# Kernel tuning notes

Measured on AMD Instinct MI355X. Metric: run time of the kernel, lower is better.

The kernel has to match this reference:

```python
import jax, jax.numpy as jnp
import numpy as np

T = 8
TAU = 2.0       # spikingjelly LIFNode default tau
VTH = 1.0       # default v_threshold
ALPHA = 2.0     # surrogate.ATan alpha
EPS = 1e-5      # BatchNorm eps


@jax.custom_vjp
def spike_fn(x):
    # Heaviside with ATan surrogate gradient
    return (x >= 0.0).astype(x.dtype)

def _spike_fwd(x):
    return (x >= 0.0).astype(x.dtype), x

def _spike_bwd(x, g):
    sg = (ALPHA / 2.0) / (1.0 + (jnp.pi / 2.0 * ALPHA * x) ** 2)
    return (g * sg,)

spike_fn.defvjp(_spike_fwd, _spike_bwd)


def lif(x_seq):
    """Multi-step LIF over leading time axis. decay_input=True, hard reset to 0, detach_reset."""
    def step(v, x):
        v = v + (x - v) / TAU            # charge
        s = spike_fn(v - VTH)            # fire (surrogate grad)
        v = v * (1.0 - jax.lax.stop_gradient(s))  # detached hard reset to v_reset=0
        return v, s
    _, s_seq = jax.lax.scan(step, jnp.zeros_like(x_seq[0]), x_seq)
    return s_seq


def conv2d(x, w, b, stride):
    y = jax.lax.conv_general_dilated(x, w, (stride, stride), 'VALID',
                                     dimension_numbers=('NCHW', 'OIHW', 'NCHW'))
    return y + b[None, :, None, None]


def batchnorm(x, g, b):
    # training-mode BN over merged (T*B, H, W) axes, matching step_mode='m' BatchNorm2d
    m = x.mean((0, 2, 3), keepdims=True)
    v = x.var((0, 2, 3), keepdims=True)
    return g[None, :, None, None] * (x - m) * jax.lax.rsqrt(v + EPS) + b[None, :, None, None]


def setup_inputs() -> dict:
    key = jax.random.key(0)
    ks = jax.random.split(key, 12)
    def w_init(k, shape):
        fan_in = int(np.prod(shape[1:]))
        return jax.random.normal(k, shape, dtype=jnp.float32) / np.sqrt(fan_in)
    x = jax.random.normal(ks[0], (128, 4, 84, 84), dtype=jnp.float32)
    return {
        'x': x,
        'conv1_w': w_init(ks[1], (32, 4, 8, 8)),  'conv1_b': jnp.zeros((32,), jnp.float32),
        'bn1_g': jnp.ones((32,), jnp.float32),    'bn1_b': jnp.zeros((32,), jnp.float32),
        'conv2_w': w_init(ks[2], (64, 32, 4, 4)), 'conv2_b': jnp.zeros((64,), jnp.float32),
        'bn2_g': jnp.ones((64,), jnp.float32),    'bn2_b': jnp.zeros((64,), jnp.float32),
        'conv3_w': w_init(ks[3], (64, 64, 3, 3)), 'conv3_b': jnp.zeros((64,), jnp.float32),
        'bn3_g': jnp.ones((64,), jnp.float32),    'bn3_b': jnp.zeros((64,), jnp.float32),
        'fc1_w': w_init(ks[4], (512, 3136)),      'fc1_b': jnp.zeros((512,), jnp.float32),
        'fco_w': w_init(ks[5], (2, 512)),         'fco_b': jnp.zeros((2,), jnp.float32),
    }


def reference(x, conv1_w, conv1_b, bn1_g, bn1_b, conv2_w, conv2_b, bn2_g, bn2_b,
              conv3_w, conv3_b, bn3_g, bn3_b, fc1_w, fc1_b, fco_w, fco_b):
    B = x.shape[0]
    # replicate input over T timesteps; fold T into batch for conv/BN (step_mode='m')
    xs = jnp.broadcast_to(x, (T,) + x.shape).reshape((T * B,) + x.shape[1:])

    h = batchnorm(conv2d(xs, conv1_w, conv1_b, 4), bn1_g, bn1_b)   # [TB,32,20,20]
    s = lif(h.reshape((T, B) + h.shape[1:]))
    h = s.reshape((T * B,) + s.shape[2:])

    h = batchnorm(conv2d(h, conv2_w, conv2_b, 2), bn2_g, bn2_b)    # [TB,64,9,9]
    s = lif(h.reshape((T, B) + h.shape[1:]))
    h = s.reshape((T * B,) + s.shape[2:])

    h = batchnorm(conv2d(h, conv3_w, conv3_b, 1), bn3_g, bn3_b)    # [TB,64,7,7]
    s = lif(h.reshape((T, B) + h.shape[1:]))                        # [T,B,64,7,7]

    feat = s.reshape(T, B, -1)                                      # [T,B,3136]
    hid = lif(jnp.einsum('tbi,oi->tbo', feat, fc1_w) + fc1_b)       # [T,B,512]
    out_seq = jnp.einsum('tbo,ko->tbk', hid, fco_w) + fco_b         # [T,B,2]
    return out_seq.mean(0)                                          # [B,2]
```

## Files before the change

### kernel.cpp

```cpp
#include <hip/hip_runtime.h>
#include <cstdint>
#include <cstddef>

#define TT 8

#define E2_ELEMS (128*64*81)
#define E3_ELEMS (128*64*49)

typedef __attribute__((ext_vector_type(8))) short short8;
typedef __attribute__((ext_vector_type(4))) float f32x4;

#define BAR_LDS() do { asm volatile("s_waitcnt lgkmcnt(0)" ::: "memory"); \
                       __builtin_amdgcn_s_barrier(); } while (0)

__device__ __forceinline__ void gld_lds16(const void* g, void* l) {
  __builtin_amdgcn_global_load_lds((const __attribute__((address_space(1))) void*)g,
                                   (__attribute__((address_space(3))) void*)l, 16, 0, 0);
}

__global__ void prep_all(const float* __restrict__ w1, const float* __restrict__ w2,
                         const float* __restrict__ w3, float* __restrict__ wT1,
                         __bf16* __restrict__ w2f, __bf16* __restrict__ w3f) {
  int i = blockIdx.x * 256 + threadIdx.x;
  if (i < 8192) {
    int oc = i >> 8, pos = i & 255;
    wT1[(oc >> 4) * 4096 + pos * 16 + (oc & 15)] = w1[oc * 256 + pos];
  } else if (i < 106496) {
    int v = i - 8192;
    int j    = v & 7;
    int oc   = (v >> 3) & 63;
    int quad = (v >> 9) & 3;
    int ksg  = (v >> 11) & 15;
    int term = v >> 15;
    int k = ksg * 32 + quad * 8 + j;
    int ci = k >> 4, kpos = k & 15;
    float w = w2[oc * 512 + ci * 16 + kpos];
    float hf = (float)(__bf16)w;
    float r1 = w - hf;
    float mf = (float)(__bf16)r1;
    float r2 = r1 - mf;
    w2f[v] = (term == 0) ? (__bf16)w : (term == 1) ? (__bf16)r1 : (__bf16)r2;
  } else if (i < 217088) {
    int v = i - 106496;
    int j    = v & 7;
    int oc   = (v >> 3) & 63;
    int quad = (v >> 9) & 3;
    int tk   = v >> 11;
    int term = tk / 18, kstep = tk % 18;
    int k = kstep * 32 + quad * 8 + j;
    int pos = k >> 6, ci = k & 63;
    float w = w3[oc * 576 + ci * 9 + pos];
    float hf = (float)(__bf16)w;
    float r1 = w - hf;
    float mf = (float)(__bf16)r1;
    float r2 = r1 - mf;
    w3f[v] = (term == 0) ? (__bf16)w : (term == 1) ? (__bf16)r1 : (__bf16)r2;
  }
}

__global__ __launch_bounds__(256) void prep_wff(const float* __restrict__ w,
                                                __bf16* __restrict__ wf) {
  __shared__ float tile[12544];
  int oc0 = blockIdx.x * 32;
  int ci0 = blockIdx.y * 8;
  int tid = threadIdx.x;
  for (int f = tid; f < 12544; f += 256) {
    int oc_l = f / 392, r = f - oc_l * 392;
    tile[f] = w[(size_t)(oc0 + oc_l) * 3136 + ci0 * 49 + r];
  }
  __syncthreads();
  int squad = (ci0 & 31) >> 3;
  int sadd  = ci0 >> 5;
  for (int g = tid; g < 1568; g += 256) {
    int pos = g >> 5, oc_l = g & 31;
    union { __bf16 h[8]; uint4 u; } T0, T1, T2;
    #pragma unroll
    for (int j = 0; j < 8; j++) {
      float wv = tile[oc_l * 392 + j * 49 + pos];
      float hf = (float)(__bf16)wv;
      float r1 = wv - hf;
      float mf = (float)(__bf16)r1;
      float r2 = r1 - mf;
      T0.h[j] = (__bf16)wv; T1.h[j] = (__bf16)r1; T2.h[j] = (__bf16)r2;
    }
    int s = pos * 2 + sadd;
    size_t b0 = (((size_t)s * 4 + squad) * 512 + oc0 + oc_l) * 8;
    *(uint4*)(wf + b0)           = T0.u;
    *(uint4*)(wf + b0 + 1605632) = T1.u;
    *(uint4*)(wf + b0 + 3211264) = T2.u;
  }
}

__global__ __launch_bounds__(128) void k_conv1(const float* __restrict__ x,
                                               const float* __restrict__ wT,
                                               const float* __restrict__ bias,
                                               float* __restrict__ out,
                                               float* __restrict__ pout) {
  __shared__ float xt[8064];
  int tid = threadIdx.x;
  int img = blockIdx.x >> 2;
  int q   = blockIdx.x & 3;
  int och = blockIdx.y;
  float4* dst = (float4*)xt;
  #pragma unroll
  for (int ci = 0; ci < 4; ci++) {
    const float4* s4 = (const float4*)(x + (size_t)img * 28224 + ci * 7056 + q * 1680);
    for (int i = tid; i < 504; i += 128) dst[ci * 504 + i] = s4[i];
  }
  __syncthreads();
  bool active = tid < 100;
  int oyl = tid / 20, ox = tid % 20;
  float acc[16];
  #pragma unroll
  for (int j = 0; j < 16; j++) acc[j] = 0.f;
  if (active) {
    int xb0 = oyl * 336 + ox * 4;
    const float* wh = wT + och * 4096;
    #pragma unroll 1
    for (int ci = 0; ci < 4; ci++) {
      #pragma unroll 1
      for (int ky = 0; ky < 8; ky++) {
        const float* xr = xt + ci * 2016 + xb0 + ky * 84;
        float4 xa  = *(const float4*)xr;
        float4 xbv = *(const float4*)(xr + 4);
        const float* wr = wh + (ci * 8 + ky) * 128;
        float xs[8] = {xa.x, xa.y, xa.z, xa.w, xbv.x, xbv.y, xbv.z, xbv.w};
        #pragma unroll
        for (int kx = 0; kx < 8; kx++) {
          #pragma unroll
          for (int j = 0; j < 16; j++)
            acc[j] = fmaf(xs[kx], wr[kx * 16 + j], acc[j]);
        }
      }
    }
  }
  __syncthreads();
  size_t obase = (size_t)img * 12800 + och * 6400 + (q * 5 + oyl) * 20 + ox;
  #pragma unroll
  for (int j = 0; j < 16; j++) {
    float v = 0.f;
    if (active) {
      v = acc[j] + bias[och * 16 + j];
      out[obase + j * 400] = v;
    }
    xt[j * 128 + tid] = v;
    xt[2048 + j * 128 + tid] = v * v;
  }
  __syncthreads();
  for (int off = 64; off > 0; off >>= 1) {
    if (tid < off) {
      #pragma unroll
      for (int j = 0; j < 16; j++) {
        xt[j * 128 + tid] += xt[j * 128 + tid + off];
        xt[2048 + j * 128 + tid] += xt[2048 + j * 128 + tid + off];
      }
    }
    __syncthreads();
  }
  if (tid < 16) {
    pout[(och * 16 + tid) * 512 + blockIdx.x] = xt[tid * 128];
    pout[16384 + (och * 16 + tid) * 512 + blockIdx.x] = xt[2048 + tid * 128];
  }
}

__global__ void k_bnfinal2(const float* __restrict__ pin, int sqoff, float n,
                           float* __restrict__ meanArr, float* __restrict__ rstdArr) {
  __shared__ float l0[256], l1[256];
  int c = blockIdx.x, tid = threadIdx.x;
  l0[tid] = pin[c * 512 + tid] + pin[c * 512 + tid + 256];
  l1[tid] = pin[sqoff + c * 512 + tid] + pin[sqoff + c * 512 + tid + 256];
  __syncthreads();
  for (int k = 128; k > 0; k >>= 1) {
    if (tid < k) { l0[tid] += l0[tid + k]; l1[tid] += l1[tid + k]; }
    __syncthreads();
  }
  if (tid == 0) {
    float m = l0[0] / n;
    float var = l1[0] / n - m * m;
    meanArr[c] = m;
    rstdArr[c] = rsqrtf(var + 1e-5f);
  }
}

__global__ void k_lif1b(const float* __restrict__ h, const float* __restrict__ mean,
                        const float* __restrict__ rstd, const float* __restrict__ g,
                        const float* __restrict__ bb, uint32_t* __restrict__ sout) {
  int idx = blockIdx.x * 256 + threadIdx.x;
  int ic = idx / 20;
  int ci = ic & 31;
  const float* hp = h + (size_t)idx * 20;
  float gm = g[ci], mm = mean[ci], rs = rstd[ci], bc = bb[ci];
  float xv[20];
  #pragma unroll
  for (int j4 = 0; j4 < 5; j4++) {
    float4 hv = ((const float4*)hp)[j4];
    xv[j4 * 4 + 0] = gm * (hv.x - mm) * rs + bc;
    xv[j4 * 4 + 1] = gm * (hv.y - mm) * rs + bc;
    xv[j4 * 4 + 2] = gm * (hv.z - mm) * rs + bc;
    xv[j4 * 4 + 3] = gm * (hv.w - mm) * rs + bc;
  }
  float v[20];
  #pragma unroll
  for (int j = 0; j < 20; j++) v[j] = 0.f;
  #pragma unroll
  for (int t = 0; t < TT; t++) {
    uint32_t w = 0;
    #pragma unroll
    for (int j = 0; j < 20; j++) {
      v[j] = v[j] + (xv[j] - v[j]) * 0.5f;
      uint32_t s = (v[j] >= 1.0f);
      w |= s << j;
      if (s) v[j] = 0.f;
    }
    sout[t * 81920 + idx] = w;
  }
}

__global__ __launch_bounds__(256) void k_conv2m(const uint32_t* __restrict__ s1b,
                                                const __bf16* __restrict__ wf,
                                                const float* __restrict__ bias,
                                                float* __restrict__ out,
                                                float* __restrict__ pout) {
  __shared__ uint32_t sp[1280];
  __shared__ uint4 wl4[3072];
  __bf16* wl = (__bf16*)wl4;
  int tid = threadIdx.x;
  int img0 = blockIdx.x * 2;
  {
    const uint32_t* src = s1b + (size_t)img0 * 640;
    for (int i = tid; i < 1280; i += 256) sp[i] = src[i];
  }
  int wave = tid >> 6, lane = tid & 63;
  int img_local = wave >> 1;
  int nh = wave & 1;
  int l15 = lane & 15, quad = lane >> 4;
  int ci_off = quad >> 1;
  int kyp = (quad & 1) * 2;
  int spb[6], sh[6];
  #pragma unroll
  for (int mt = 0; mt < 6; mt++) {
    int px = mt * 16 + l15;
    if (px > 80) px = 80;
    int oy = px / 9, ox = px - oy * 9;
    sh[mt]  = ox * 2;
    spb[mt] = img_local * 640 + ci_off * 20 + oy * 2 + kyp;
  }
  f32x4 acc[6][2];
  #pragma unroll
  for (int mt = 0; mt < 6; mt++)
    #pragma unroll
    for (int nt = 0; nt < 2; nt++) acc[mt][nt] = (f32x4){0.f, 0.f, 0.f, 0.f};

  for (int kc = 0; kc < 4; kc++) {
    __syncthreads();
    for (int o = tid * 8; o < 24576; o += 2048) {
      int tk = o >> 11;
      int term = tk >> 2, ksl = tk & 3;
      const __bf16* src = wf + (((term * 16 + kc * 4 + ksl)) << 11) + (o & 2047);
      gld_lds16(src, wl + o);
    }
    __syncthreads();
    #pragma unroll
    for (int ks = 0; ks < 4; ks++) {
      int ksg = kc * 4 + ks;
      short8 a[6];
      #pragma unroll
      for (int mt = 0; mt < 6; mt++) {
        uint32_t w0 = sp[spb[mt] + ksg * 40];
        uint32_t w1 = sp[spb[mt] + ksg * 40 + 1];
        uint32_t n0 = (w0 >> sh[mt]) & 15u;
        uint32_t n1 = (w1 >> sh[mt]) & 15u;
        union { uint32_t u[4]; short8 v; } A;
        A.u[0] = ((n0 & 1u) ? 0x3F80u : 0u) | ((n0 & 2u) ? 0x3F800000u : 0u);
        A.u[1] = ((n0 & 4u) ? 0x3F80u : 0u) | ((n0 & 8u) ? 0x3F800000u : 0u);
        A.u[2] = ((n1 & 1u) ? 0x3F80u : 0u) | ((n1 & 2u) ? 0x3F800000u : 0u);
        A.u[3] = ((n1 & 4u) ? 0x3F80u : 0u) | ((n1 & 8u) ? 0x3F800000u : 0u);
        a[mt] = A.v;
      }
      #pragma unroll
      for (int term = 0; term < 3; term++) {
        int fb = ((term * 4 + ks) << 11) + (quad << 9);
        #pragma unroll
        for (int nt = 0; nt < 2; nt++) {
          short8 b = *(const short8*)(wl + fb + ((((nh << 1) | nt) << 4) + l15) * 8);
          #pragma unroll
          for (int mt = 0; mt < 6; mt++)
            acc[mt][nt] = __builtin_amdgcn_mfma_f32_16x16x32_bf16(a[mt], b, acc[mt][nt], 0, 0, 0);
        }
      }
    }
  }
  float sl[2], sl2[2];
  #pragma unroll
  for (int nt = 0; nt < 2; nt++) {
    sl[nt] = 0.f; sl2[nt] = 0.f;
    int oc = nh * 32 + nt * 16 + l15;
    float bv = bias[oc];
    float* op = out + ((size_t)(img0 + img_local) * 64 + oc) * 81;
    #pragma unroll
    for (int mt = 0; mt < 6; mt++) {
      int pxr = mt * 16 + quad * 4;
      #pragma unroll
      for (int r = 0; r < 4; r++) {
        int px = pxr + r;
        if (px < 81) {
          float v = acc[mt][nt][r] + bv;
          op[px] = v;
          sl[nt] += v; sl2[nt] += v * v;
        }
      }
    }
  }
  __syncthreads();
  float* sred = (float*)wl4;
  #pragma unroll
  for (int nt = 0; nt < 2; nt++) {
    int oc = nh * 32 + nt * 16 + l15;
    int idx = oc * 8 + img_local * 4 + quad;
    sred[idx] = sl[nt];
    sred[512 + idx] = sl2[nt];
  }
  __syncthreads();
  if (tid < 64) {
    float s = 0.f, s2 = 0.f;
    #pragma unroll
    for (int k = 0; k < 8; k++) { s += sred[tid * 8 + k]; s2 += sred[512 + tid * 8 + k]; }
    pout[tid * 512 + blockIdx.x] = s;
    pout[32768 + tid * 512 + blockIdx.x] = s2;
  }
}

__global__ __launch_bounds__(256) void k_lifb2T(const float* __restrict__ h,
                                                const float* __restrict__ mean,
                                                const float* __restrict__ rstd,
                                                const float* __restrict__ g,
                                                const float* __restrict__ bb,
                                                uint32_t* __restrict__ s2T) {
  __shared__ uint32_t sb[288];
  int b = blockIdx.x, half = blockIdx.y;
  int tid = threadIdx.x;
  int c1 = half * 32 + tid / 9, py1 = tid % 9;
  bool has2 = tid < 32;
  int r2 = tid + 256;
  int c2i = half * 32 + r2 / 9, py2 = r2 % 9;
  float gm1 = g[c1], mm1 = mean[c1], rs1 = rstd[c1], bc1 = bb[c1];
  float gm2 = 0.f, mm2 = 0.f, rs2 = 0.f, bc2 = 0.f;
  if (has2) { gm2 = g[c2i]; mm2 = mean[c2i]; rs2 = rstd[c2i]; bc2 = bb[c2i]; }
  float v1[9], v2[9];
  #pragma unroll
  for (int j = 0; j < 9; j++) { v1[j] = 0.f; v2[j] = 0.f; }
  size_t base1 = ((size_t)b * 64 + c1) * 81 + py1 * 9;
  size_t base2 = has2 ? ((size_t)b * 64 + c2i) * 81 + py2 * 9 : base1;
  float c1v[9], c2v[9];
  {
    const float* hp = h;
    #pragma unroll
    for (int j = 0; j < 9; j++) c1v[j] = hp[base1 + j];
    if (has2) {
      #pragma unroll
      for (int j = 0; j < 9; j++) c2v[j] = hp[base2 + j];
    }
  }
  #pragma unroll 1
  for (int t = 0; t < TT; t++) {
    float n1v[9], n2v[9];
    if (t < TT - 1) {
      const float* hp = h + (size_t)(t + 1) * E2_ELEMS;
      #pragma unroll
      for (int j = 0; j < 9; j++) n1v[j] = hp[base1 + j];
      if (has2) {
        #pragma unroll
        for (int j = 0; j < 9; j++) n2v[j] = hp[base2 + j];
      }
    }
    uint32_t w = 0;
    #pragma unroll
    for (int j = 0; j < 9; j++) {
      float xv = gm1 * (c1v[j] - mm1) * rs1 + bc1;
      v1[j] = v1[j] + (xv - v1[j]) * 0.5f;
      uint32_t s = (v1[j] >= 1.0f);
      w |= s << j;
      if (s) v1[j] = 0.f;
    }
    sb[tid] = w;
    if (has2) {
      uint32_t w2 = 0;
      #pragma unroll
      for (int j = 0; j < 9; j++) {
        float xv = gm2 * (c2v[j] - mm2) * rs2 + bc2;
        v2[j] = v2[j] + (xv - v2[j]) * 0.5f;
        uint32_t s = (v2[j] >= 1.0f);
        w2 |= s << j;
        if (s) v2[j] = 0.f;
      }
      sb[r2] = w2;
    }
    BAR_LDS();
    if (tid < 81) {
      int r = tid / 9, cpix = tid - r * 9;
      uint32_t wo = 0;
      #pragma unroll
      for (int ci = 0; ci < 32; ci++)
        wo |= ((sb[ci * 9 + r] >> cpix) & 1u) << ci;
      s2T[(size_t)(t * 128 + b) * 162 + tid * 2 + half] = wo;
    }
    BAR_LDS();
    if (t < TT - 1) {
      #pragma unroll
      for (int j = 0; j < 9; j++) c1v[j] = n1v[j];
      if (has2) {
        #pragma unroll
        for (int j = 0; j < 9; j++) c2v[j] = n2v[j];
      }
    }
  }
}

__global__ __launch_bounds__(256) void k_conv3m(const uint32_t* __restrict__ s2T,
                                                const __bf16* __restrict__ wf,
                                                const float* __restrict__ bias,
                                                float* __restrict__ out,
                                                float* __restrict__ pout) {
  __shared__ uint32_t sp[324];
  __shared__ uint4 wl4[4608];
  __bf16* wl = (__bf16*)wl4;
  int tid = threadIdx.x;
  int img0 = blockIdx.x * 2;
  {
    const uint32_t* src = s2T + (size_t)img0 * 162;
    for (int i = tid; i < 324; i += 256) sp[i] = src[i];
  }
  int wave = tid >> 6, lane = tid & 63;
  int img_local = wave >> 1, nh = wave & 1;
  int l15 = lane & 15, quad = lane >> 4;
  int qsh = quad * 8;
  int base[4];
  #pragma unroll
  for (int mt = 0; mt < 4; mt++) {
    int px = mt * 16 + l15;
    if (px > 48) px = 48;
    int oy = px / 7, ox = px - oy * 7;
    base[mt] = img_local * 162 + (oy * 9 + ox) * 2;
  }
  f32x4 acc[4][2];
  #pragma unroll
  for (int mt = 0; mt < 4; mt++)
    #pragma unroll
    for (int nt = 0; nt < 2; nt++) acc[mt][nt] = (f32x4){0.f, 0.f, 0.f, 0.f};

  #pragma unroll
  for (int kc = 0; kc < 3; kc++) {
    __syncthreads();
    #pragma unroll
    for (int it = 0; it < 18; it++) {
      const __bf16* s = wf + (((it / 6) * 18 + kc * 6 + (it % 6)) << 11) + tid * 8;
      gld_lds16(s, wl + (it << 11) + tid * 8);
    }
    __syncthreads();
    #pragma unroll
    for (int ksl = 0; ksl < 6; ksl++) {
      int kstep = kc * 6 + ksl;
      int pos = kstep >> 1, cihalf = kstep & 1;
      int ky = pos / 3, kx = pos % 3;
      short8 a[4];
      #pragma unroll
      for (int mt = 0; mt < 4; mt++) {
        uint32_t word = sp[base[mt] + (ky * 9 + kx) * 2 + cihalf];
        uint32_t byt = (word >> qsh) & 255u;
        union { uint32_t u[4]; short8 v; } A;
        A.u[0] = ((byt & 1u)  ? 0x3F80u : 0u) | ((byt & 2u)   ? 0x3F800000u : 0u);
        A.u[1] = ((byt & 4u)  ? 0x3F80u : 0u) | ((byt & 8u)   ? 0x3F800000u : 0u);
        A.u[2] = ((byt & 16u) ? 0x3F80u : 0u) | ((byt & 32u)  ? 0x3F800000u : 0u);
        A.u[3] = ((byt & 64u) ? 0x3F80u : 0u) | ((byt & 128u) ? 0x3F800000u : 0u);
        a[mt] = A.v;
      }
      #pragma unroll
      for (int term = 0; term < 3; term++) {
        int fb = ((term * 6 + ksl) << 11) + (quad << 9);
        #pragma unroll
        for (int nt = 0; nt < 2; nt++) {
          short8 b = *(const short8*)(wl + fb + ((((nh << 1) | nt) << 4) + l15) * 8);
          #pragma unroll
          for (int mt = 0; mt < 4; mt++)
            acc[mt][nt] = __builtin_amdgcn_mfma_f32_16x16x32_bf16(a[mt], b, acc[mt][nt], 0, 0, 0);
        }
      }
    }
  }
  float sl[2], sl2[2];
  #pragma unroll
  for (int nt = 0; nt < 2; nt++) {
    sl[nt] = 0.f; sl2[nt] = 0.f;
    int oc = nh * 32 + nt * 16 + l15;
    float bv = bias[oc];
    float* op = out + ((size_t)(img0 + img_local) * 64 + oc) * 49;
    #pragma unroll
    for (int mt = 0; mt < 4; mt++) {
      int pxr = mt * 16 + quad * 4;
      #pragma unroll
      for (int r = 0; r < 4; r++) {
        int px = pxr + r;
        if (px < 49) {
          float v = acc[mt][nt][r] + bv;
          op[px] = v;
          sl[nt] += v; sl2[nt] += v * v;
        }
      }
    }
  }
  __syncthreads();
  float* sred = (float*)wl4;
  #pragma unroll
  for (int nt = 0; nt < 2; nt++) {
    int oc = nh * 32 + nt * 16 + l15;
    int idx = oc * 8 + img_local * 4 + quad;
    sred[idx] = sl[nt];
    sred[512 + idx] = sl2[nt];
  }
  __syncthreads();
  if (tid < 64) {
    float s = 0.f, s2 = 0.f;
    #pragma unroll
    for (int k = 0; k < 8; k++) { s += sred[tid * 8 + k]; s2 += sred[512 + tid * 8 + k]; }
    pout[tid * 512 + blockIdx.x] = s;
    pout[32768 + tid * 512 + blockIdx.x] = s2;
  }
}

__global__ __launch_bounds__(256) void k_lifb3T(const float* __restrict__ h,
                                                const float* __restrict__ mean,
                                                const float* __restrict__ rstd,
                                                const float* __restrict__ g,
                                                const float* __restrict__ bb,
                                                uint32_t* __restrict__ s3T) {
  __shared__ uint32_t sb[224];
  int b = blockIdx.x, half = blockIdx.y;
  int tid = threadIdx.x;
  bool active = tid < 224;
  int row = active ? tid : 0;
  int c = half * 32 + row / 7, py = row % 7;
  float gm = g[c], mm = mean[c], rs = rstd[c], bc = bb[c];
  float v[7];
  #pragma unroll
  for (int j = 0; j < 7; j++) v[j] = 0.f;
  size_t base = ((size_t)b * 64 + c) * 49 + py * 7;
  float cv[7];
  if (active) {
    #pragma unroll
    for (int j = 0; j < 7; j++) cv[j] = h[base + j];
  }
  #pragma unroll 1
  for (int t = 0; t < TT; t++) {
    float nv[7];
    if (active && t < TT - 1) {
      const float* hp = h + (size_t)(t + 1) * E3_ELEMS;
      #pragma unroll
      for (int j = 0; j < 7; j++) nv[j] = hp[base + j];
    }
    if (active) {
      uint32_t w = 0;
      #pragma unroll
      for (int j = 0; j < 7; j++) {
        float xv = gm * (cv[j] - mm) * rs + bc;
        v[j] = v[j] + (xv - v[j]) * 0.5f;
        uint32_t s = (v[j] >= 1.0f);
        w |= s << j;
        if (s) v[j] = 0.f;
      }
      sb[tid] = w;
    }
    BAR_LDS();
    if (tid < 49) {
      int py2 = tid / 7, px = tid - py2 * 7;
      uint32_t wo = 0;
      #pragma unroll
      for (int ci = 0; ci < 32; ci++)
        wo |= ((sb[ci * 7 + py2] >> px) & 1u) << ci;
      s3T[(size_t)(t * 128 + b) * 98 + tid * 2 + half] = wo;
    }
    BAR_LDS();
    if (active && t < TT - 1) {
      #pragma unroll
      for (int j = 0; j < 7; j++) cv[j] = nv[j];
    }
  }
}

__global__ __launch_bounds__(256) void k_fc1m(const uint32_t* __restrict__ s3T,
                                              const __bf16* __restrict__ wf,
                                              float* __restrict__ f1) {
  __shared__ uint32_t aS[6272];
  int tid = threadIdx.x;
  int row0 = blockIdx.x * 64;
  int oc0  = blockIdx.y * 16;
  {
    const uint32_t* src = s3T + (size_t)row0 * 98;
    for (int i = tid; i < 6272; i += 256) aS[i] = src[i];
  }
  __syncthreads();
  int wave = tid >> 6, lane = tid & 63;
  int l15 = lane & 15, quad = lane >> 4;
  int qsh = quad * 8;
  f32x4 acc[4];
  #pragma unroll
  for (int mt = 0; mt < 4; mt++) acc[mt] = (f32x4){0.f, 0.f, 0.f, 0.f};
  int nIter = (wave < 2) ? 25 : 24;
  #pragma unroll 2
  for (int i = 0; i < nIter; i++) {
    int ks = i * 4 + wave;
    short8 a[4];
    #pragma unroll
    for (int mt = 0; mt < 4; mt++) {
      uint32_t word = aS[(mt * 16 + l15) * 98 + ks];
      uint32_t byt = (word >> qsh) & 255u;
      union { uint32_t u[4]; short8 v; } A;
      A.u[0] = ((byt & 1u)  ? 0x3F80u : 0u) | ((byt & 2u)   ? 0x3F800000u : 0u);
      A.u[1] = ((byt & 4u)  ? 0x3F80u : 0u) | ((byt & 8u)   ? 0x3F800000u : 0u);
      A.u[2] = ((byt & 16u) ? 0x3F80u : 0u) | ((byt & 32u)  ? 0x3F800000u : 0u);
      A.u[3] = ((byt & 64u) ? 0x3F80u : 0u) | ((byt & 128u) ? 0x3F800000u : 0u);
      a[mt] = A.v;
    }
    #pragma unroll
    for (int term = 0; term < 3; term++) {
      size_t fb = ((size_t)((term * 98 + ks) * 4 + quad) * 512 + oc0 + l15) * 8;
      short8 b = *(const short8*)(wf + fb);
      #pragma unroll
      for (int mt = 0; mt < 4; mt++)
        acc[mt] = __builtin_amdgcn_mfma_f32_16x16x32_bf16(a[mt], b, acc[mt], 0, 0, 0);
    }
  }
  __syncthreads();
  float* red = (float*)aS;
  #pragma unroll
  for (int mt = 0; mt < 4; mt++)
    #pragma unroll
    for (int r = 0; r < 4; r++)
      red[(wave * 64 + lane) * 17 + mt * 4 + r] = acc[mt][r];
  __syncthreads();
  #pragma unroll
  for (int k = 0; k < 4; k++) {
    int oi = tid + k * 256;
    int row_l = oi >> 4, oc_l = oi & 15;
    int mt = row_l >> 4, rem = row_l & 15;
    int q2 = rem >> 2, r = rem & 3;
    int ln = q2 * 16 + oc_l;
    float s = red[(0 * 64 + ln) * 17 + mt * 4 + r];
    s += red[(1 * 64 + ln) * 17 + mt * 4 + r];
    s += red[(2 * 64 + ln) * 17 + mt * 4 + r];
    s += red[(3 * 64 + ln) * 17 + mt * 4 + r];
    f1[(size_t)(row0 + row_l) * 512 + oc0 + oc_l] = s;
  }
}

__global__ __launch_bounds__(256) void k_fc1fco(const float* __restrict__ f1,
                                                const float* __restrict__ bias,
                                                const float* __restrict__ w,
                                                const float* __restrict__ fcob,
                                                float* __restrict__ out) {
  int b = blockIdx.x, tid = threadIdx.x;
  int o0 = tid, o1 = tid + 256;
  float bv0 = bias[o0], bv1 = bias[o1];
  float w00 = w[o0], w10 = w[512 + o0];
  float w01 = w[o1], w11 = w[512 + o1];
  float x0[TT], x1[TT];
  #pragma unroll
  for (int t = 0; t < TT; t++) {
    x0[t] = f1[(size_t)(t * 128 + b) * 512 + o0];
    x1[t] = f1[(size_t)(t * 128 + b) * 512 + o1];
  }
  float v0 = 0.f, v1 = 0.f;
  float a0 = 0.f, a1 = 0.f;
  #pragma unroll
  for (int t = 0; t < TT; t++) {
    float s0 = x0[t] + bv0;
    v0 = v0 + (s0 - v0) * 0.5f;
    bool sp0 = (v0 >= 1.0f);
    if (sp0) v0 = 0.f;
    float s1 = x1[t] + bv1;
    v1 = v1 + (s1 - v1) * 0.5f;
    bool sp1 = (v1 >= 1.0f);
    if (sp1) v1 = 0.f;
    if (sp0) { a0 += w00; a1 += w10; }
    if (sp1) { a0 += w01; a1 += w11; }
  }
  __shared__ float l0[256], l1[256];
  l0[tid] = a0; l1[tid] = a1; __syncthreads();
  for (int k = 128; k > 0; k >>= 1) {
    if (tid < k) { l0[tid] += l0[tid + k]; l1[tid] += l1[tid + k]; }
    __syncthreads();
  }
  if (tid == 0) {
    out[b * 2 + 0] = l0[0] * 0.125f + fcob[0];
    out[b * 2 + 1] = l1[0] * 0.125f + fcob[1];
  }
}

extern "C" void kernel_launch(void* const* d_in, const int* in_sizes, int n_in,
                              void* d_out, int out_size, void* d_ws, size_t ws_size,
                              hipStream_t stream) {
  const float* x    = (const float*)d_in[0];
  const float* c1w  = (const float*)d_in[1];
  const float* c1b  = (const float*)d_in[2];
  const float* bn1g = (const float*)d_in[3];
  const float* bn1b = (const float*)d_in[4];
  const float* c2w  = (const float*)d_in[5];
  const float* c2b  = (const float*)d_in[6];
  const float* bn2g = (const float*)d_in[7];
  const float* bn2b = (const float*)d_in[8];
  const float* c3w  = (const float*)d_in[9];
  const float* c3b  = (const float*)d_in[10];
  const float* bn3g = (const float*)d_in[11];
  const float* bn3b = (const float*)d_in[12];
  const float* fc1w = (const float*)d_in[13];
  const float* fc1b = (const float*)d_in[14];
  const float* fcow = (const float*)d_in[15];
  const float* fcob = (const float*)d_in[16];
  float* out = (float*)d_out;

  char* ws = (char*)d_ws;
  float*    h1     = (float*)(ws + 0);
  uint32_t* s1bits = (uint32_t*)(ws + 6553600);
  float*    h2     = (float*)(ws + 19660800);
  float*    h3     = (float*)(ws + 46202880);
  __bf16*   w2f    = (__bf16*)(ws + 60882944);
  __bf16*   w3f    = (__bf16*)(ws + 61079552);
  uint32_t* s2T    = (uint32_t*)(ws + 61300736);
  float*    wT1    = (float*)(ws + 62390272);
  float*    st     = (float*)(ws + 64880640);
  __bf16*   wff    = (__bf16*)(ws + 67108864);
  float*    f1sum  = (float*)(ws + 76742656);
  uint32_t* s3T    = (uint32_t*)(ws + 85131264);
  float*    bnpart = (float*)(ws + 85532672);

  prep_all   <<<848, 256, 0, stream>>>(c1w, c2w, c3w, wT1, w2f, w3f);
  prep_wff   <<<dim3(16, 8), 256, 0, stream>>>(fc1w, wff);
  k_conv1    <<<dim3(512, 2), 128, 0, stream>>>(x, wT1, c1b, h1, bnpart);
  k_bnfinal2 <<<32, 256, 0, stream>>>(bnpart, 16384, 51200.f, st, st + 32);
  k_lif1b    <<<320, 256, 0, stream>>>(h1, st, st + 32, bn1g, bn1b, s1bits);

  k_conv2m   <<<512, 256, 0, stream>>>(s1bits, w2f, c2b, h2, bnpart);
  k_bnfinal2 <<<64, 256, 0, stream>>>(bnpart, 32768, 82944.f, st + 64, st + 128);
  k_lifb2T   <<<dim3(128, 2), 256, 0, stream>>>(h2, st + 64, st + 128, bn2g, bn2b, s2T);

  k_conv3m   <<<512, 256, 0, stream>>>(s2T, w3f, c3b, h3, bnpart);
  k_bnfinal2 <<<64, 256, 0, stream>>>(bnpart, 32768, 50176.f, st + 192, st + 256);
  k_lifb3T   <<<dim3(128, 2), 256, 0, stream>>>(h3, st + 192, st + 256, bn3g, bn3b, s3T);

  k_fc1m     <<<dim3(16, 32), 256, 0, stream>>>(s3T, wff, f1sum);
  k_fc1fco   <<<128, 256, 0, stream>>>(f1sum, fc1b, fcow, fcob, out);
}
```

Measured before the change: 247.0 us.

## Move conv1 to split-bf16 MFMA and fold BN finalization into conv kernels

Conv1 is rewritten from scalar FP32 FMAs into an implicit GEMM on bf16 MFMA. Input and weights are each split into three bf16 terms and combined over eight MFMA products to keep roughly FP32 accuracy. The separate BN-statistics finalize kernels are removed: each conv kernel bumps an atomic counter, and the last block to finish reduces the partial sums into mean and rstd. prep_wff is merged into prep_all, which also resets the counters, cutting five launches in total. The trade-offs are extra LDS for the split input, MFMA work on padded pixels, and a serialized tail reduction in the last block.

```diff
diff --git a/kernel.cpp b/kernel.cpp
--- a/kernel.cpp
+++ b/kernel.cpp
@@ -8,6 +8,7 @@
 #define E3_ELEMS (128*64*49)
 
 typedef __attribute__((ext_vector_type(8))) short short8;
+typedef __attribute__((ext_vector_type(4))) short short4v;
 typedef __attribute__((ext_vector_type(4))) float f32x4;
 
 #define BAR_LDS() do { asm volatile("s_waitcnt lgkmcnt(0)" ::: "memory"); \
@@ -18,15 +19,70 @@
                                    (__attribute__((address_space(3))) void*)l, 16, 0, 0);
 }
 
-__global__ void prep_all(const float* __restrict__ w1, const float* __restrict__ w2,
-                         const float* __restrict__ w3, float* __restrict__ wT1,
-                         __bf16* __restrict__ w2f, __bf16* __restrict__ w3f) {
-  int i = blockIdx.x * 256 + threadIdx.x;
-  if (i < 8192) {
-    int oc = i >> 8, pos = i & 255;
-    wT1[(oc >> 4) * 4096 + pos * 16 + (oc & 15)] = w1[oc * 256 + pos];
-  } else if (i < 106496) {
-    int v = i - 8192;
+__device__ __forceinline__ void split3(float v, ushort& h, ushort& m, ushort& l) {
+  union { __bf16 b; ushort u; } H, M, L;
+  H.b = (__bf16)v; float r1 = v - (float)H.b;
+  M.b = (__bf16)r1; float r2 = r1 - (float)M.b;
+  L.b = (__bf16)r2;
+  h = H.u; m = M.u; l = L.u;
+}
+
+__device__ __forceinline__ short8 ld8(const ushort* p) {
+  union { short4v h[2]; short8 v; } U;
+  U.h[0] = *(const short4v*)(p);
+  U.h[1] = *(const short4v*)(p + 4);
+  return U.v;
+}
+
+__global__ __launch_bounds__(256) void prep_all(const float* __restrict__ w1,
+                                                const float* __restrict__ w2,
+                                                const float* __restrict__ w3,
+                                                const float* __restrict__ wfc,
+                                                __bf16* __restrict__ w1f,
+                                                __bf16* __restrict__ w2f,
+                                                __bf16* __restrict__ w3f,
+                                                __bf16* __restrict__ wff,
+                                                uint32_t* __restrict__ cnt) {
+  __shared__ float tile[12544];
+  int bxx = blockIdx.x;
+  int tid = threadIdx.x;
+  if (bxx == 0 && tid < 3) cnt[tid] = 0;
+
+  if (bxx >= 912) {
+    int bx2 = bxx - 912;
+    int oc0 = (bx2 >> 3) * 32;
+    int ci0 = (bx2 & 7) * 8;
+    for (int f = tid; f < 12544; f += 256) {
+      int oc_l = f / 392, r = f - oc_l * 392;
+      tile[f] = wfc[(size_t)(oc0 + oc_l) * 3136 + ci0 * 49 + r];
+    }
+    __syncthreads();
+    int squad = (ci0 & 31) >> 3;
+    int sadd  = ci0 >> 5;
+    for (int g = tid; g < 1568; g += 256) {
+      int pos = g >> 5, oc_l = g & 31;
+      union { __bf16 h[8]; uint4 u; } T0, T1, T2;
+      #pragma unroll
+      for (int j = 0; j < 8; j++) {
+        float wv = tile[oc_l * 392 + j * 49 + pos];
+        float hf = (float)(__bf16)wv;
+        float r1 = wv - hf;
+        float mf = (float)(__bf16)r1;
+        float r2 = r1 - mf;
+        T0.h[j] = (__bf16)wv; T1.h[j] = (__bf16)r1; T2.h[j] = (__bf16)r2;
+      }
+      int s = pos * 2 + sadd;
+      size_t b0 = (((size_t)s * 4 + squad) * 512 + oc0 + oc_l) * 8;
+      *(uint4*)(wff + b0)           = T0.u;
+      *(uint4*)(wff + b0 + 1605632) = T1.u;
+      *(uint4*)(wff + b0 + 3211264) = T2.u;
+    }
+    return;
+  }
+
+  int i = bxx * 256 + tid;
+  if (i < 98304) {
+    int v = i;
     int j    = v & 7;
     int oc   = (v >> 3) & 63;
     int quad = (v >> 9) & 3;
@@ -40,8 +96,8 @@
     float mf = (float)(__bf16)r1;
     float r2 = r1 - mf;
     w2f[v] = (term == 0) ? (__bf16)w : (term == 1) ? (__bf16)r1 : (__bf16)r2;
-  } else if (i < 217088) {
-    int v = i - 106496;
+  } else if (i < 208896) {
+    int v = i - 98304;
     int j    = v & 7;
     int oc   = (v >> 3) & 63;
     int quad = (v >> 9) & 3;
@@ -55,130 +111,156 @@
     float mf = (float)(__bf16)r1;
     float r2 = r1 - mf;
     w3f[v] = (term == 0) ? (__bf16)w : (term == 1) ? (__bf16)r1 : (__bf16)r2;
-  }
-}
-
-__global__ __launch_bounds__(256) void prep_wff(const float* __restrict__ w,
-                                                __bf16* __restrict__ wf) {
-  __shared__ float tile[12544];
-  int oc0 = blockIdx.x * 32;
-  int ci0 = blockIdx.y * 8;
+  } else {
+    int v = i - 208896;
+    int j    = v & 7;
+    int oc   = (v >> 3) & 31;
+    int quad = (v >> 8) & 3;
+    int ks   = (v >> 10) & 7;
+    int term = v >> 13;
+    int k = ks * 32 + quad * 8 + j;
+    float w = w1[oc * 256 + k];
+    float hf = (float)(__bf16)w;
+    float r1 = w - hf;
+    float mf = (float)(__bf16)r1;
+    float r2 = r1 - mf;
+    w1f[v] = (term == 0) ? (__bf16)w : (term == 1) ? (__bf16)r1 : (__bf16)r2;
+  }
+}
+
+__global__ __launch_bounds__(128) void k_conv1m(const float* __restrict__ x,
+                                                const __bf16* __restrict__ w1f,
+                                                const float* __restrict__ bias,
+                                                float* __restrict__ out,
+                                                float* __restrict__ pout,
+                                                uint32_t* __restrict__ cnt,
+                                                float* __restrict__ meanArr,
+                                                float* __restrict__ rstdArr) {
+  __shared__ ushort xs[24192];
+  __shared__ uint32_t flag;
   int tid = threadIdx.x;
-  for (int f = tid; f < 12544; f += 256) {
-    int oc_l = f / 392, r = f - oc_l * 392;
-    tile[f] = w[(size_t)(oc0 + oc_l) * 3136 + ci0 * 49 + r];
-  }
-  __syncthreads();
-  int squad = (ci0 & 31) >> 3;
-  int sadd  = ci0 >> 5;
-  for (int g = tid; g < 1568; g += 256) {
-    int pos = g >> 5, oc_l = g & 31;
-    union { __bf16 h[8]; uint4 u; } T0, T1, T2;
-    #pragma unroll
-    for (int j = 0; j < 8; j++) {
-      float wv = tile[oc_l * 392 + j * 49 + pos];
-      float hf = (float)(__bf16)wv;
-      float r1 = wv - hf;
-      float mf = (float)(__bf16)r1;
-      float r2 = r1 - mf;
-      T0.h[j] = (__bf16)wv; T1.h[j] = (__bf16)r1; T2.h[j] = (__bf16)r2;
-    }
-    int s = pos * 2 + sadd;
-    size_t b0 = (((size_t)s * 4 + squad) * 512 + oc0 + oc_l) * 8;
-    *(uint4*)(wf + b0)           = T0.u;
-    *(uint4*)(wf + b0 + 1605632) = T1.u;
-    *(uint4*)(wf + b0 + 3211264) = T2.u;
-  }
-}
-
-__global__ __launch_bounds__(128) void k_conv1(const float* __restrict__ x,
-                                               const float* __restrict__ wT,
-                                               const float* __restrict__ bias,
-                                               float* __restrict__ out,
-                                               float* __restrict__ pout) {
-  __shared__ float xt[8064];
-  int tid = threadIdx.x;
-  int img = blockIdx.x >> 2;
-  int q   = blockIdx.x & 3;
-  int och = blockIdx.y;
-  float4* dst = (float4*)xt;
-  #pragma unroll
-  for (int ci = 0; ci < 4; ci++) {
-    const float4* s4 = (const float4*)(x + (size_t)img * 28224 + ci * 7056 + q * 1680);
-    for (int i = tid; i < 504; i += 128) dst[ci * 504 + i] = s4[i];
-  }
-  __syncthreads();
-  bool active = tid < 100;
-  int oyl = tid / 20, ox = tid % 20;
-  float acc[16];
-  #pragma unroll
-  for (int j = 0; j < 16; j++) acc[j] = 0.f;
-  if (active) {
-    int xb0 = oyl * 336 + ox * 4;
-    const float* wh = wT + och * 4096;
-    #pragma unroll 1
-    for (int ci = 0; ci < 4; ci++) {
-      #pragma unroll 1
-      for (int ky = 0; ky < 8; ky++) {
-        const float* xr = xt + ci * 2016 + xb0 + ky * 84;
-        float4 xa  = *(const float4*)xr;
-        float4 xbv = *(const float4*)(xr + 4);
-        const float* wr = wh + (ci * 8 + ky) * 128;
-        float xs[8] = {xa.x, xa.y, xa.z, xa.w, xbv.x, xbv.y, xbv.z, xbv.w};
-        #pragma unroll
-        for (int kx = 0; kx < 8; kx++) {
-          #pragma unroll
-          for (int j = 0; j < 16; j++)
-            acc[j] = fmaf(xs[kx], wr[kx * 16 + j], acc[j]);
-        }
-      }
-    }
-  }
-  __syncthreads();
-  size_t obase = (size_t)img * 12800 + och * 6400 + (q * 5 + oyl) * 20 + ox;
-  #pragma unroll
-  for (int j = 0; j < 16; j++) {
-    float v = 0.f;
-    if (active) {
-      v = acc[j] + bias[och * 16 + j];
-      out[obase + j * 400] = v;
-    }
-    xt[j * 128 + tid] = v;
-    xt[2048 + j * 128 + tid] = v * v;
-  }
-  __syncthreads();
-  for (int off = 64; off > 0; off >>= 1) {
-    if (tid < off) {
-      #pragma unroll
-      for (int j = 0; j < 16; j++) {
-        xt[j * 128 + tid] += xt[j * 128 + tid + off];
-        xt[2048 + j * 128 + tid] += xt[2048 + j * 128 + tid + off];
-      }
-    }
-    __syncthreads();
-  }
-  if (tid < 16) {
-    pout[(och * 16 + tid) * 512 + blockIdx.x] = xt[tid * 128];
-    pout[16384 + (och * 16 + tid) * 512 + blockIdx.x] = xt[2048 + tid * 128];
-  }
-}
-
-__global__ void k_bnfinal2(const float* __restrict__ pin, int sqoff, float n,
-                           float* __restrict__ meanArr, float* __restrict__ rstdArr) {
-  __shared__ float l0[256], l1[256];
-  int c = blockIdx.x, tid = threadIdx.x;
-  l0[tid] = pin[c * 512 + tid] + pin[c * 512 + tid + 256];
-  l1[tid] = pin[sqoff + c * 512 + tid] + pin[sqoff + c * 512 + tid + 256];
-  __syncthreads();
-  for (int k = 128; k > 0; k >>= 1) {
-    if (tid < k) { l0[tid] += l0[tid + k]; l1[tid] += l1[tid + k]; }
-    __syncthreads();
-  }
-  if (tid == 0) {
-    float m = l0[0] / n;
-    float var = l1[0] / n - m * m;
-    meanArr[c] = m;
-    rstdArr[c] = rsqrtf(var + 1e-5f);
+  int bx = blockIdx.x;
+  int img = bx >> 2, q = bx & 3;
+  const float* xb = x + (size_t)img * 28224 + q * 1680;
+  for (int f = tid; f < 2016; f += 128) {
+    int ci = f / 504, rr = f - ci * 504;
+    int row = rr / 21, c4 = rr - row * 21;
+    float4 v4 = *(const float4*)(xb + ci * 7056 + row * 84 + c4 * 4);
+    union { ushort s[4]; uint2 u; } H, M, L;
+    float vv[4] = {v4.x, v4.y, v4.z, v4.w};
+    #pragma unroll
+    for (int j = 0; j < 4; j++) split3(vv[j], H.s[j], M.s[j], L.s[j]);
+    int eo = ci * 2016 + row * 84 + c4 * 4;
+    *(uint2*)(xs + eo)         = H.u;
+    *(uint2*)(xs + 8064 + eo)  = M.u;
+    *(uint2*)(xs + 16128 + eo) = L.u;
+  }
+  __syncthreads();
+  int nh = tid >> 6, lane = tid & 63;
+  int l15 = lane & 15, quad = lane >> 4;
+  int aoff[7];
+  #pragma unroll
+  for (int mt = 0; mt < 7; mt++) {
+    int px = mt * 16 + l15; if (px > 99) px = 99;
+    int oy = px / 20, ox = px - oy * 20;
+    aoff[mt] = oy * 336 + ox * 4;
+  }
+  f32x4 acc[7];
+  #pragma unroll
+  for (int mt = 0; mt < 7; mt++) acc[mt] = (f32x4){0.f, 0.f, 0.f, 0.f};
+  const __bf16* wpb = w1f + quad * 256 + (nh * 16 + l15) * 8;
+  for (int ks = 0; ks < 8; ks++) {
+    const __bf16* wp = wpb + ks * 1024;
+    short8 bh = *(const short8*)(wp);
+    short8 bm = *(const short8*)(wp + 8192);
+    short8 bl = *(const short8*)(wp + 16384);
+    int pair = ks * 4 + quad;
+    int e0 = (pair >> 3) * 2016 + (pair & 7) * 84;
+    short8 ah[7], am[7], al[7];
+    #pragma unroll
+    for (int mt = 0; mt < 7; mt++) {
+      int e = e0 + aoff[mt];
+      ah[mt] = ld8(xs + e);
+      am[mt] = ld8(xs + 8064 + e);
+      al[mt] = ld8(xs + 16128 + e);
+    }
+    #pragma unroll
+    for (int mt = 0; mt < 7; mt++)
+      acc[mt] = __builtin_amdgcn_mfma_f32_16x16x32_bf16(ah[mt], bh, acc[mt], 0, 0, 0);
+    #pragma unroll
+    for (int mt = 0; mt < 7; mt++)
+      acc[mt] = __builtin_amdgcn_mfma_f32_16x16x32_bf16(ah[mt], bm, acc[mt], 0, 0, 0);
+    #pragma unroll
+    for (int mt = 0; mt < 7; mt++)
+      acc[mt] = __builtin_amdgcn_mfma_f32_16x16x32_bf16(am[mt], bh, acc[mt], 0, 0, 0);
+    #pragma unroll
+    for (int mt = 0; mt < 7; mt++)
+      acc[mt] = __builtin_amdgcn_mfma_f32_16x16x32_bf16(am[mt], bm, acc[mt], 0, 0, 0);
+    #pragma unroll
+    for (int mt = 0; mt < 7; mt++)
+      acc[mt] = __builtin_amdgcn_mfma_f32_16x16x32_bf16(ah[mt], bl, acc[mt], 0, 0, 0);
+    #pragma unroll
+    for (int mt = 0; mt < 7; mt++)
+      acc[mt] = __builtin_amdgcn_mfma_f32_16x16x32_bf16(al[mt], bh, acc[mt], 0, 0, 0);
+    #pragma unroll
+    for (int mt = 0; mt < 7; mt++)
+      acc[mt] = __builtin_amdgcn_mfma_f32_16x16x32_bf16(am[mt], bl, acc[mt], 0, 0, 0);
+    #pragma unroll
+    for (int mt = 0; mt < 7; mt++)
+      acc[mt] = __builtin_amdgcn_mfma_f32_16x16x32_bf16(al[mt], bm, acc[mt], 0, 0, 0);
+  }
+  int oc = nh * 16 + l15;
+  float bv = bias[oc];
+  float sl = 0.f, sl2 = 0.f;
+  float* op = out + (size_t)img * 12800 + oc * 400 + q * 100;
+  #pragma unroll
+  for (int mt = 0; mt < 7; mt++) {
+    int pxb = mt * 16 + quad * 4;
+    #pragma unroll
+    for (int r = 0; r < 4; r++) {
+      int px = pxb + r;
+      if (px < 100) {
+        float v = acc[mt][r] + bv;
+        op[px] = v;
+        sl += v; sl2 += v * v;
+      }
+    }
+  }
+  __syncthreads();
+  float* sred = (float*)xs;
+  sred[oc * 4 + quad] = sl;
+  sred[128 + oc * 4 + quad] = sl2;
+  __syncthreads();
+  if (tid < 32) {
+    float s  = sred[tid*4] + sred[tid*4+1] + sred[tid*4+2] + sred[tid*4+3];
+    float s2 = sred[128+tid*4] + sred[128+tid*4+1] + sred[128+tid*4+2] + sred[128+tid*4+3];
+    pout[tid * 512 + bx] = s;
+    pout[16384 + tid * 512 + bx] = s2;
+  }
+  __threadfence();
+  __syncthreads();
+  if (tid == 0) flag = (atomicAdd(cnt, 1u) == 511u) ? 1u : 0u;
+  __syncthreads();
+  if (flag) {
+    __threadfence();
+    int c = tid >> 2, s4 = tid & 3;
+    float s = 0.f, s2 = 0.f;
+    #pragma unroll 4
+    for (int k = 0; k < 128; k++) {
+      s  += pout[c * 512 + s4 * 128 + k];
+      s2 += pout[16384 + c * 512 + s4 * 128 + k];
+    }
+    __syncthreads();
+    sred[tid] = s; sred[128 + tid] = s2;
+    __syncthreads();
+    if (tid < 32) {
+      float ts  = sred[tid*4] + sred[tid*4+1] + sred[tid*4+2] + sred[tid*4+3];
+      float ts2 = sred[128+tid*4] + sred[128+tid*4+1] + sred[128+tid*4+2] + sred[128+tid*4+3];
+      float m = ts / 51200.f;
+      float var = ts2 / 51200.f - m * m;
+      meanArr[tid] = m;
+      rstdArr[tid] = rsqrtf(var + 1e-5f);
+    }
   }
 }
 
@@ -220,9 +302,13 @@
                                                 const __bf16* __restrict__ wf,
                                                 const float* __restrict__ bias,
                                                 float* __restrict__ out,
-                                                float* __restrict__ pout) {
+                                                float* __restrict__ pout,
+                                                uint32_t* __restrict__ cnt,
+                                                float* __restrict__ meanArr,
+                                                float* __restrict__ rstdArr) {
   __shared__ uint32_t sp[1280];
   __shared__ uint4 wl4[3072];
+  __shared__ uint32_t flag;
   __bf16* wl = (__bf16*)wl4;
   int tid = threadIdx.x;
   int img0 = blockIdx.x * 2;
@@ -327,6 +413,32 @@
     for (int k = 0; k < 8; k++) { s += sred[tid * 8 + k]; s2 += sred[512 + tid * 8 + k]; }
     pout[tid * 512 + blockIdx.x] = s;
     pout[32768 + tid * 512 + blockIdx.x] = s2;
+  }
+  __threadfence();
+  __syncthreads();
+  if (tid == 0) flag = (atomicAdd(cnt, 1u) == 511u) ? 1u : 0u;
+  __syncthreads();
+  if (flag) {
+    __threadfence();
+    int c = tid >> 2, s4 = tid & 3;
+    float s = 0.f, s2 = 0.f;
+    #pragma unroll 4
+    for (int k = 0; k < 128; k++) {
+      s  += pout[c * 512 + s4 * 128 + k];
+      s2 += pout[32768 + c * 512 + s4 * 128 + k];
+    }
+    __syncthreads();
+    float* red = (float*)wl4;
+    red[tid] = s; red[256 + tid] = s2;
+    __syncthreads();
+    if (tid < 64) {
+      float ts  = red[tid*4] + red[tid*4+1] + red[tid*4+2] + red[tid*4+3];
+      float ts2 = red[256+tid*4] + red[256+tid*4+1] + red[256+tid*4+2] + red[256+tid*4+3];
+      float m = ts / 82944.f;
+      float var = ts2 / 82944.f - m * m;
+      meanArr[tid] = m;
+      rstdArr[tid] = rsqrtf(var + 1e-5f);
+    }
   }
 }
 
@@ -420,9 +532,13 @@
                                                 const __bf16* __restrict__ wf,
                                                 const float* __restrict__ bias,
                                                 float* __restrict__ out,
-                                                float* __restrict__ pout) {
+                                                float* __restrict__ pout,
+                                                uint32_t* __restrict__ cnt,
+                                                float* __restrict__ meanArr,
+                                                float* __restrict__ rstdArr) {
   __shared__ uint32_t sp[324];
   __shared__ uint4 wl4[4608];
+  __shared__ uint32_t flag;
   __bf16* wl = (__bf16*)wl4;
   int tid = threadIdx.x;
   int img0 = blockIdx.x * 2;
@@ -524,6 +640,32 @@
     for (int k = 0; k < 8; k++) { s += sred[tid * 8 + k]; s2 += sred[512 + tid * 8 + k]; }
     pout[tid * 512 + blockIdx.x] = s;
     pout[32768 + tid * 512 + blockIdx.x] = s2;
+  }
+  __threadfence();
+  __syncthreads();
+  if (tid == 0) flag = (atomicAdd(cnt, 1u) == 511u) ? 1u : 0u;
+  __syncthreads();
+  if (flag) {
+    __threadfence();
+    int c = tid >> 2, s4 = tid & 3;
+    float s = 0.f, s2 = 0.f;
+    #pragma unroll 4
+    for (int k = 0; k < 128; k++) {
+      s  += pout[c * 512 + s4 * 128 + k];
+      s2 += pout[32768 + c * 512 + s4 * 128 + k];
+    }
+    __syncthreads();
+    float* red = (float*)wl4;
+    red[tid] = s; red[256 + tid] = s2;
+    __syncthreads();
+    if (tid < 64) {
+      float ts  = red[tid*4] + red[tid*4+1] + red[tid*4+2] + red[tid*4+3];
+      float ts2 = red[256+tid*4] + red[256+tid*4+1] + red[256+tid*4+2] + red[256+tid*4+3];
+      float m = ts / 50176.f;
+      float var = ts2 / 50176.f - m * m;
+      meanArr[tid] = m;
+      rstdArr[tid] = rsqrtf(var + 1e-5f);
+    }
   }
 }
 
@@ -725,27 +867,25 @@
   __bf16*   w2f    = (__bf16*)(ws + 60882944);
   __bf16*   w3f    = (__bf16*)(ws + 61079552);
   uint32_t* s2T    = (uint32_t*)(ws + 61300736);
-  float*    wT1    = (float*)(ws + 62390272);
+  __bf16*   w1f    = (__bf16*)(ws + 62390272);
   float*    st     = (float*)(ws + 64880640);
+  uint32_t* cnt    = (uint32_t*)(ws + 64885760);
   __bf16*   wff    = (__bf16*)(ws + 67108864);
   float*    f1sum  = (float*)(ws + 76742656);
   uint32_t* s3T    = (uint32_t*)(ws + 85131264);
   float*    bnpart = (float*)(ws + 85532672);
 
-  prep_all   <<<848, 256, 0, stream>>>(c1w, c2w, c3w, wT1, w2f, w3f);
-  prep_wff   <<<dim3(16, 8), 256, 0, stream>>>(fc1w, wff);
-  k_conv1    <<<dim3(512, 2), 128, 0, stream>>>(x, wT1, c1b, h1, bnpart);
-  k_bnfinal2 <<<32, 256, 0, stream>>>(bnpart, 16384, 51200.f, st, st + 32);
-  k_lif1b    <<<320, 256, 0, stream>>>(h1, st, st + 32, bn1g, bn1b, s1bits);
-
-  k_conv2m   <<<512, 256, 0, stream>>>(s1bits, w2f, c2b, h2, bnpart);
-  k_bnfinal2 <<<64, 256, 0, stream>>>(bnpart, 32768, 82944.f, st + 64, st + 128);
-  k_lifb2T   <<<dim3(128, 2), 256, 0, stream>>>(h2, st + 64, st + 128, bn2g, bn2b, s2T);
-
-  k_conv3m   <<<512, 256, 0, stream>>>(s2T, w3f, c3b, h3, bnpart);
-  k_bnfinal2 <<<64, 256, 0, stream>>>(bnpart, 32768, 50176.f, st + 192, st + 256);
-  k_lifb3T   <<<dim3(128, 2), 256, 0, stream>>>(h3, st + 192, st + 256, bn3g, bn3b, s3T);
-
-  k_fc1m     <<<dim3(16, 32), 256, 0, stream>>>(s3T, wff, f1sum);
-  k_fc1fco   <<<128, 256, 0, stream>>>(f1sum, fc1b, fcow, fcob, out);
-}
+  prep_all <<<1040, 256, 0, stream>>>(c1w, c2w, c3w, fc1w, w1f, w2f, w3f, wff, cnt);
+
+  k_conv1m <<<512, 128, 0, stream>>>(x, w1f, c1b, h1, bnpart, cnt + 0, st, st + 32);
+  k_lif1b  <<<320, 256, 0, stream>>>(h1, st, st + 32, bn1g, bn1b, s1bits);
+
+  k_conv2m <<<512, 256, 0, stream>>>(s1bits, w2f, c2b, h2, bnpart, cnt + 1, st + 64, st + 128);
+  k_lifb2T <<<dim3(128, 2), 256, 0, stream>>>(h2, st + 64, st + 128, bn2g, bn2b, s2T);
+
+  k_conv3m <<<512, 256, 0, stream>>>(s2T, w3f, c3b, h3, bnpart, cnt + 2, st + 192, st + 256);
+  k_lifb3T <<<dim3(128, 2), 256, 0, stream>>>(h3, st + 192, st + 256, bn3g, bn3b, s3T);
+
+  k_fc1m   <<<dim3(16, 32), 256, 0, stream>>>(s3T, wff, f1sum);
+  k_fc1fco <<<128, 256, 0, stream>>>(f1sum, fc1b, fcow, fcob, out);
+}
```

Result: slower. 410.5 us (+66.2%).
